# Performance work log

Measured on AMD Instinct MI355X. Metric: run time of the kernel, lower is better.

## Reference

```python
import jax, jax.numpy as jnp
import numpy as np

N_NODES = 100000


def setup_inputs() -> dict:
    key = jax.random.key(0)
    ks = jax.random.split(key, 8)
    N, E, D_IN, D_OUT = N_NODES, 1600000, 64, 64
    return {
        "emb_src": jax.random.normal(ks[0], (N, D_IN), dtype=jnp.float32),
        "emb_dst": jax.random.normal(ks[1], (N, D_IN), dtype=jnp.float32),
        "edge_weight": jax.random.uniform(ks[2], (E,), dtype=jnp.float32),
        "W": jax.random.normal(ks[3], (D_IN, D_OUT), dtype=jnp.float32) / np.sqrt(D_IN),
        "b": jnp.zeros((D_OUT,), dtype=jnp.float32),
        "src_idx": jax.random.randint(ks[4], (E,), 0, N),
        "dst_idx": jax.random.randint(ks[5], (E,), 0, N),
        "user_indices": jax.random.randint(ks[6], (N,), 0, 1000000),
        "labels": jax.random.randint(ks[7], (N,), 0, 2),
        "perm": jnp.arange(N),
    }


def reference(emb_src, emb_dst, edge_weight, W, b, src_idx, dst_idx, user_indices, labels, perm):
    # DGL update_all(u_mul_e('embedding','weight','m'), sum('m','ft')):
    # gather source embeddings, scale by edge weight, scatter-sum into dst.
    msgs = emb_src[src_idx] * edge_weight[:, None]            # [E, D]
    ft = jax.ops.segment_sum(msgs, dst_idx, num_segments=N_NODES)  # [N, D]
    # aggregate == 'SUM': self embedding + aggregated neighborhood
    h = emb_dst + ft                                          # [N, D]
    # per-row np.where(itemlist == dst_ID) matching -> permutation gather
    users = user_indices[perm]
    labs = labels[perm]
    # last layer: tanh(Linear(h)) (dropout p=0 is identity)
    item_embeddings = jnp.tanh(h @ W + b)                     # [N, D_OUT]
    return item_embeddings, users, labs
```

## Files before the change

### kernel.cpp

```cpp
#include <hip/hip_runtime.h>
#include <hip/hip_fp16.h>

#define D 64
#define NQ (D / 4)
#define NB 512
#define NPB 196
#define LOCAL_BITS 8
#define LOCAL_MASK 255
#define SCAN_W 512
#define CAP 4096
#define CAPB 3584
#define SCATTER_BLKS 256
#define FRONT_BLKS 2048

#define HACC_STRIDE 17
#define SMEM_BYTES (D * D * 4 + NPB * HACC_STRIDE * 16)

__device__ __forceinline__ float fast_tanh(float x) {
    float e = __expf(2.0f * x);
    return 1.0f - 2.0f / (e + 1.0f);
}

struct f8 { float4 a, b; };

__global__ __launch_bounds__(512) void init_cursor_kernel(int* __restrict__ cursor)
{
    int t = threadIdx.x;
    if (t < NB) cursor[t] = t * CAPB;
}

__global__ __launch_bounds__(1024) void front2_kernel(
    const int* __restrict__ src_idx,
    const int* __restrict__ dst_idx,
    const float* __restrict__ edge_weight,
    int* __restrict__ cursor,
    int2* __restrict__ payload,
    const int* __restrict__ user_indices,
    const int* __restrict__ labels,
    const int* __restrict__ perm,
    const float* __restrict__ emb_src,
    __half* __restrict__ emb_h,
    float* __restrict__ users_out,
    float* __restrict__ labs_out,
    int n_edges, int chunk, int n_nodes)
{
    const int tid = threadIdx.x;

    if (blockIdx.x < SCATTER_BLKS) {
        __shared__ int hist[NB];
        __shared__ int blockbase[NB];
        __shared__ int cur[NB];
        int lo = blockIdx.x * chunk;
        int hi = min(n_edges, lo + chunk);

        for (int i = tid; i < NB; i += 1024) { hist[i] = 0; cur[i] = 0; }
        __syncthreads();
        for (int e = lo + tid; e < hi; e += 1024)
            atomicAdd(&hist[(unsigned)dst_idx[e] / NPB], 1);
        __syncthreads();
        for (int i = tid; i < NB; i += 1024) {
            int c = hist[i];
            blockbase[i] = c ? atomicAdd(&cursor[i], c) : 0;
        }
        __syncthreads();
        for (int e = lo + tid; e < hi; e += 1024) {
            int d = dst_idx[e];
            unsigned bkt = (unsigned)d / NPB;
            int pos = blockbase[bkt] + atomicAdd(&cur[bkt], 1);
            if (pos < (int)(bkt + 1) * CAPB)
                payload[pos] = make_int2((src_idx[e] << LOCAL_BITS) | (d - (int)bkt * NPB),
                                         __float_as_int(edge_weight[e]));
        }
    } else {
        const int nblk = gridDim.x - SCATTER_BLKS;
        const int gstride = nblk * 1024;
        const int t0 = (blockIdx.x - SCATTER_BLKS) * 1024 + tid;
        for (int i = t0; i < n_nodes; i += gstride) {
            int p = perm[i];
            users_out[i] = (float)user_indices[p];
            labs_out[i]  = (float)labels[p];
        }
        const int n_cvt = n_nodes * NQ;
        for (int i = t0; i < n_cvt; i += gstride) {
            float4 v = reinterpret_cast<const float4*>(emb_src)[i];
            __half2 a, b;
            a.x = __float2half_rn(v.x); a.y = __float2half_rn(v.y);
            b.x = __float2half_rn(v.z); b.y = __float2half_rn(v.w);
            uint2 u;
            u.x = *reinterpret_cast<unsigned*>(&a);
            u.y = *reinterpret_cast<unsigned*>(&b);
            reinterpret_cast<uint2*>(emb_h)[i] = u;
        }
    }
}

template <bool USE_H, bool FIXED_BASE>
__global__ __launch_bounds__(1024, 8) void fused_gather_gemm_kernel(
    const float* __restrict__ emb_src,
    const __half* __restrict__ emb_h,
    const float* __restrict__ emb_dst,
    const float* __restrict__ Wmat,
    const float* __restrict__ bias,
    const int2* __restrict__ payload,
    const int* __restrict__ base_or_cursor,
    const int* __restrict__ counts,
    float* __restrict__ out,
    int n_nodes)
{
    __shared__ __align__(16) char smem[SMEM_BYTES];
    float*  Ws     = reinterpret_cast<float*>(smem);
    float4* Hacc   = reinterpret_cast<float4*>(smem + D * D * 4);
    int2*   sedges = reinterpret_cast<int2*>(smem + D * D * 4);
    int*    cnt    = reinterpret_cast<int*>(smem + D * D * 4 + CAP * 8);
    int*    scn    = cnt + 256;
    int*    cur    = scn + 256;

    const int tid = threadIdx.x;
    const int b   = blockIdx.x;
    int start, end;
    if constexpr (FIXED_BASE) {
        start = b * CAPB;
        end   = min(base_or_cursor[b], start + CAPB);
    } else {
        start = base_or_cursor[b];
        end   = start + counts[b];
    }

    const int g8 = tid >> 3;
    const int q8 = tid & 7;
    const float4* esrc = reinterpret_cast<const float4*>(emb_src);

    reinterpret_cast<float4*>(Ws)[tid] = reinterpret_cast<const float4*>(Wmat)[tid];

    float4 accA[2], accB[2];
    #pragma unroll
    for (int k = 0; k < 2; ++k) {
        accA[k] = make_float4(0.f, 0.f, 0.f, 0.f);
        accB[k] = make_float4(0.f, 0.f, 0.f, 0.f);
    }

    for (int cbase = start; cbase < end; cbase += CAP) {
        const int m = min(end - cbase, CAP);

        for (int i = tid; i < 256; i += 1024) { cnt[i] = 0; cur[i] = 0; }
        __syncthreads();

        int2 pe[4];
        #pragma unroll
        for (int j = 0; j < 4; ++j) {
            int i = cbase + tid + j * 1024;
            if (tid + j * 1024 < m) {
                pe[j] = payload[i];
                atomicAdd(&cnt[pe[j].x & LOCAL_MASK], 1);
            }
        }
        __syncthreads();

        if (tid < 256) scn[tid] = cnt[tid];
        __syncthreads();
        #pragma unroll
        for (int d = 1; d < 256; d <<= 1) {
            int x = 0;
            if (tid < 256 && tid >= d) x = scn[tid - d];
            __syncthreads();
            if (tid < 256) scn[tid] += x;
            __syncthreads();
        }
        if (tid < 256) scn[tid] -= cnt[tid];
        __syncthreads();

        #pragma unroll
        for (int j = 0; j < 4; ++j) {
            if (tid + j * 1024 < m) {
                int local = pe[j].x & LOCAL_MASK;
                int pos = scn[local] + atomicAdd(&cur[local], 1);
                sedges[pos] = pe[j];
            }
        }
        __syncthreads();

        #pragma unroll
        for (int k = 0; k < 2; ++k) {
            int n = g8 + 128 * k;
            if (n < NPB) {
                int mm = cnt[n];
                int bs = scn[n];
                if (mm <= 0) continue;
                int lim = mm - 1;
                float4 aA = accA[k], aB = accB[k];

                if constexpr (USE_H) {
                    int2 e0 = sedges[bs];
                    int2 e1 = sedges[bs + min(1, lim)];
                    int2 e2 = sedges[bs + min(2, lim)];
                    int2 e3 = sedges[bs + min(3, lim)];
                    uint4 u0 = *reinterpret_cast<const uint4*>(
                        emb_h + ((size_t)((unsigned)e0.x >> LOCAL_BITS) << 6) + (q8 << 3));
                    uint4 u1 = *reinterpret_cast<const uint4*>(
                        emb_h + ((size_t)((unsigned)e1.x >> LOCAL_BITS) << 6) + (q8 << 3));
                    uint4 u2 = *reinterpret_cast<const uint4*>(
                        emb_h + ((size_t)((unsigned)e2.x >> LOCAL_BITS) << 6) + (q8 << 3));
                    uint4 u3 = *reinterpret_cast<const uint4*>(
                        emb_h + ((size_t)((unsigned)e3.x >> LOCAL_BITS) << 6) + (q8 << 3));

                    for (int j = 0; j < mm; j += 4) {
                        int jn = j + 4;
                        int2 f0 = sedges[bs + min(jn,     lim)];
                        int2 f1 = sedges[bs + min(jn + 1, lim)];
                        int2 f2 = sedges[bs + min(jn + 2, lim)];
                        int2 f3 = sedges[bs + min(jn + 3, lim)];
                        uint4 w0v = *reinterpret_cast<const uint4*>(
                            emb_h + ((size_t)((unsigned)f0.x >> LOCAL_BITS) << 6) + (q8 << 3));
                        uint4 w1v = *reinterpret_cast<const uint4*>(
                            emb_h + ((size_t)((unsigned)f1.x >> LOCAL_BITS) << 6) + (q8 << 3));
                        uint4 w2v = *reinterpret_cast<const uint4*>(
                            emb_h + ((size_t)((unsigned)f2.x >> LOCAL_BITS) << 6) + (q8 << 3));
                        uint4 w3v = *reinterpret_cast<const uint4*>(
                            emb_h + ((size_t)((unsigned)f3.x >> LOCAL_BITS) << 6) + (q8 << 3));

                        float w0 = __int_as_float(e0.y);
                        float w1 = (j + 1 < mm) ? __int_as_float(e1.y) : 0.f;
                        float w2 = (j + 2 < mm) ? __int_as_float(e2.y) : 0.f;
                        float w3 = (j + 3 < mm) ? __int_as_float(e3.y) : 0.f;
                        {
                            union { uint4 u; __half2 h2[4]; } c0{u0}, c1{u1}, c2{u2}, c3{u3};
                            float2 p00 = __half22float2(c0.h2[0]), p01 = __half22float2(c0.h2[1]);
                            float2 p02 = __half22float2(c0.h2[2]), p03 = __half22float2(c0.h2[3]);
                            float2 p10 = __half22float2(c1.h2[0]), p11 = __half22float2(c1.h2[1]);
                            float2 p12 = __half22float2(c1.h2[2]), p13 = __half22float2(c1.h2[3]);
                            float2 p20 = __half22float2(c2.h2[0]), p21 = __half22float2(c2.h2[1]);
                            float2 p22 = __half22float2(c2.h2[2]), p23 = __half22float2(c2.h2[3]);
                            float2 p30 = __half22float2(c3.h2[0]), p31 = __half22float2(c3.h2[1]);
                            float2 p32 = __half22float2(c3.h2[2]), p33 = __half22float2(c3.h2[3]);
                            aA.x += p00.x * w0 + p10.x * w1 + p20.x * w2 + p30.x * w3;
                            aA.y += p00.y * w0 + p10.y * w1 + p20.y * w2 + p30.y * w3;
                            aA.z += p01.x * w0 + p11.x * w1 + p21.x * w2 + p31.x * w3;
                            aA.w += p01.y * w0 + p11.y * w1 + p21.y * w2 + p31.y * w3;
                            aB.x += p02.x * w0 + p12.x * w1 + p22.x * w2 + p32.x * w3;
                            aB.y += p02.y * w0 + p12.y * w1 + p22.y * w2 + p32.y * w3;
                            aB.z += p03.x * w0 + p13.x * w1 + p23.x * w2 + p33.x * w3;
                            aB.w += p03.y * w0 + p13.y * w1 + p23.y * w2 + p33.y * w3;
                        }
                        e0 = f0; e1 = f1; e2 = f2; e3 = f3;
                        u0 = w0v; u1 = w1v; u2 = w2v; u3 = w3v;
                    }
                } else {
                    for (int j = 0; j < mm; j += 4) {
                        int2 e0 = sedges[bs + j];
                        int2 e1 = sedges[bs + min(j + 1, lim)];
                        int2 e2 = sedges[bs + min(j + 2, lim)];
                        int2 e3 = sedges[bs + min(j + 3, lim)];
                        const float4* p0 = esrc + (size_t)((unsigned)e0.x >> LOCAL_BITS) * NQ + (q8 << 1);
                        const float4* p1 = esrc + (size_t)((unsigned)e1.x >> LOCAL_BITS) * NQ + (q8 << 1);
                        const float4* p2 = esrc + (size_t)((unsigned)e2.x >> LOCAL_BITS) * NQ + (q8 << 1);
                        const float4* p3 = esrc + (size_t)((unsigned)e3.x >> LOCAL_BITS) * NQ + (q8 << 1);
                        float4 a0 = p0[0], b0 = p0[1], a1 = p1[0], b1 = p1[1];
                        float4 a2 = p2[0], b2 = p2[1], a3 = p3[0], b3 = p3[1];
                        float w0 = __int_as_float(e0.y);
                        float w1 = (j + 1 < mm) ? __int_as_float(e1.y) : 0.f;
                        float w2 = (j + 2 < mm) ? __int_as_float(e2.y) : 0.f;
                        float w3 = (j + 3 < mm) ? __int_as_float(e3.y) : 0.f;
                        aA.x += a0.x * w0 + a1.x * w1 + a2.x * w2 + a3.x * w3;
                        aA.y += a0.y * w0 + a1.y * w1 + a2.y * w2 + a3.y * w3;
                        aA.z += a0.z * w0 + a1.z * w1 + a2.z * w2 + a3.z * w3;
                        aA.w += a0.w * w0 + a1.w * w1 + a2.w * w2 + a3.w * w3;
                        aB.x += b0.x * w0 + b1.x * w1 + b2.x * w2 + b3.x * w3;
                        aB.y += b0.y * w0 + b1.y * w1 + b2.y * w2 + b3.y * w3;
                        aB.z += b0.z * w0 + b1.z * w1 + b2.z * w2 + b3.z * w3;
                        aB.w += b0.w * w0 + b1.w * w1 + b2.w * w2 + b3.w * w3;
                    }
                }
                accA[k] = aA; accB[k] = aB;
            }
        }
        __syncthreads();
    }

    const int node0 = b * NPB;
    #pragma unroll
    for (int k = 0; k < 2; ++k) {
        int n = g8 + 128 * k;
        if (n < NPB) {
            int node = node0 + n;
            float4 d0 = make_float4(0.f, 0.f, 0.f, 0.f);
            float4 d1 = make_float4(0.f, 0.f, 0.f, 0.f);
            if (node < n_nodes) {
                const float4* ed = reinterpret_cast<const float4*>(emb_dst)
                                 + (size_t)node * NQ + (q8 << 1);
                d0 = ed[0]; d1 = ed[1];
            }
            float4 aA = accA[k], aB = accB[k];
            aA.x += d0.x; aA.y += d0.y; aA.z += d0.z; aA.w += d0.w;
            aB.x += d1.x; aB.y += d1.y; aB.z += d1.z; aB.w += d1.w;
            Hacc[n * HACC_STRIDE + (q8 << 1)]     = aA;
            Hacc[n * HACC_STRIDE + (q8 << 1) + 1] = aB;
        }
    }
    __syncthreads();

    const int g = tid >> 4;
    const int q = tid & 15;
    const float4* Ws4 = reinterpret_cast<const float4*>(Ws);
    float4 bv = reinterpret_cast<const float4*>(bias)[q];
    #pragma unroll
    for (int k = 0; k < 4; ++k) {
        int n = g + 64 * k;
        int node = node0 + n;
        if (n < NPB && node < n_nodes) {
            float4 a = make_float4(0.f, 0.f, 0.f, 0.f);
            #pragma unroll 4
            for (int kk = 0; kk < 16; ++kk) {
                float4 hv = Hacc[n * HACC_STRIDE + kk];
                float4 w0 = Ws4[(4 * kk + 0) * 16 + q];
                float4 w1 = Ws4[(4 * kk + 1) * 16 + q];
                float4 w2 = Ws4[(4 * kk + 2) * 16 + q];
                float4 w3 = Ws4[(4 * kk + 3) * 16 + q];
                a.x += hv.x * w0.x + hv.y * w1.x + hv.z * w2.x + hv.w * w3.x;
                a.y += hv.x * w0.y + hv.y * w1.y + hv.z * w2.y + hv.w * w3.y;
                a.z += hv.x * w0.z + hv.y * w1.z + hv.z * w2.z + hv.w * w3.z;
                a.w += hv.x * w0.w + hv.y * w1.w + hv.z * w2.w + hv.w * w3.w;
            }
            float4 o;
            o.x = fast_tanh(a.x + bv.x);
            o.y = fast_tanh(a.y + bv.y);
            o.z = fast_tanh(a.z + bv.z);
            o.w = fast_tanh(a.w + bv.w);
            reinterpret_cast<float4*>(out)[(size_t)node * NQ + q] = o;
        }
    }
}

__global__ __launch_bounds__(256) void meta_kernel(
    const int* __restrict__ user_indices,
    const int* __restrict__ labels,
    const int* __restrict__ perm,
    const float* __restrict__ emb_src,
    __half* __restrict__ emb_h,
    float* __restrict__ users_out,
    float* __restrict__ labs_out,
    int* __restrict__ counts,
    int n_zero,
    int n_nodes)
{
    const int stride = gridDim.x * blockDim.x;
    int t0 = blockIdx.x * blockDim.x + threadIdx.x;
    if (counts)
        for (int i = t0; i < n_zero; i += stride) counts[i] = 0;
    for (int i = t0; i < n_nodes; i += stride) {
        int p = perm[i];
        users_out[i] = (float)user_indices[p];
        labs_out[i]  = (float)labels[p];
    }
    if (emb_h) {
        const int n_cvt = n_nodes * NQ;
        for (int i = t0; i < n_cvt; i += stride) {
            float4 v = reinterpret_cast<const float4*>(emb_src)[i];
            __half2 a, b;
            a.x = __float2half_rn(v.x); a.y = __float2half_rn(v.y);
            b.x = __float2half_rn(v.z); b.y = __float2half_rn(v.w);
            uint2 u;
            u.x = *reinterpret_cast<unsigned*>(&a);
            u.y = *reinterpret_cast<unsigned*>(&b);
            reinterpret_cast<uint2*>(emb_h)[i] = u;
        }
    }
}

__global__ __launch_bounds__(1024) void hist_bucket_kernel(
    const int* __restrict__ dst_idx,
    int* __restrict__ counts,
    int n_edges, int chunk)
{
    __shared__ int hist[NB];
    for (int i = threadIdx.x; i < NB; i += 1024) hist[i] = 0;
    __syncthreads();
    int lo = blockIdx.x * chunk;
    int hi = min(n_edges, lo + chunk);
    for (int e = lo + threadIdx.x; e < hi; e += 1024)
        atomicAdd(&hist[(unsigned)dst_idx[e] / NPB], 1);
    __syncthreads();
    for (int i = threadIdx.x; i < NB; i += 1024)
        if (hist[i]) atomicAdd(&counts[i], hist[i]);
}

__global__ __launch_bounds__(SCAN_W) void scan_small_kernel(
    const int* __restrict__ counts,
    int* __restrict__ base,
    int* __restrict__ cursor,
    int nb)
{
    __shared__ int s[SCAN_W];
    int t = threadIdx.x;
    int v = (t < nb) ? counts[t] : 0;
    s[t] = v;
    __syncthreads();
    #pragma unroll
    for (int d = 1; d < SCAN_W; d <<= 1) {
        int x = (t >= d) ? s[t - d] : 0;
        __syncthreads();
        s[t] += x;
        __syncthreads();
    }
    if (t < nb) { base[t] = s[t] - v; cursor[t] = s[t] - v; }
}

__global__ __launch_bounds__(1024) void scatter_bucket_kernel(
    const int* __restrict__ src_idx,
    const int* __restrict__ dst_idx,
    const float* __restrict__ edge_weight,
    int* __restrict__ cursor,
    int2* __restrict__ payload,
    int n_edges, int chunk)
{
    __shared__ int hist[NB];
    __shared__ int blockbase[NB];
    __shared__ int cur[NB];
    const int tid = threadIdx.x;
    int lo = blockIdx.x * chunk;
    int hi = min(n_edges, lo + chunk);

    for (int i = tid; i < NB; i += 1024) { hist[i] = 0; cur[i] = 0; }
    __syncthreads();
    for (int e = lo + tid; e < hi; e += 1024)
        atomicAdd(&hist[(unsigned)dst_idx[e] / NPB], 1);
    __syncthreads();
    for (int i = tid; i < NB; i += 1024) {
        int c = hist[i];
        blockbase[i] = c ? atomicAdd(&cursor[i], c) : 0;
    }
    __syncthreads();
    for (int e = lo + tid; e < hi; e += 1024) {
        int d = dst_idx[e];
        unsigned bkt = (unsigned)d / NPB;
        int pos = blockbase[bkt] + atomicAdd(&cur[bkt], 1);
        payload[pos] = make_int2((src_idx[e] << LOCAL_BITS) | (d - (int)bkt * NPB),
                                 __float_as_int(edge_weight[e]));
    }
}

__global__ __launch_bounds__(256) void init_h_kernel(
    const float* __restrict__ emb_dst, float* __restrict__ h, int n_nodes)
{
    const int stride = gridDim.x * blockDim.x;
    const int total4 = n_nodes * NQ;
    for (int i = blockIdx.x * blockDim.x + threadIdx.x; i < total4; i += stride)
        reinterpret_cast<float4*>(h)[i] = reinterpret_cast<const float4*>(emb_dst)[i];
}

__global__ __launch_bounds__(256) void scatter_kernel(
    const float* __restrict__ emb_src,
    const float* __restrict__ edge_weight,
    const int* __restrict__ src_idx,
    const int* __restrict__ dst_idx,
    float* __restrict__ h,
    int n_edges)
{
    int t = blockIdx.x * blockDim.x + threadIdx.x;
    if (t >= n_edges * NQ) return;
    int e = t >> 4;
    int q = t & 15;
    int s = src_idx[e];
    int d = dst_idx[e];
    float w = edge_weight[e];
    float4 v = reinterpret_cast<const float4*>(emb_src)[(size_t)s * NQ + q];
    float* p = h + (size_t)d * D + q * 4;
    atomicAdd(p + 0, v.x * w);
    atomicAdd(p + 1, v.y * w);
    atomicAdd(p + 2, v.z * w);
    atomicAdd(p + 3, v.w * w);
}

__global__ __launch_bounds__(256, 4) void gemm_tanh_kernel(
    float* __restrict__ h,
    const float* __restrict__ W,
    const float* __restrict__ b,
    int n_nodes)
{
    __shared__ float Ws[D * D];
    __shared__ float Hs[64 * D];

    const int tid = threadIdx.x;

    for (int i = tid; i < D * D / 4; i += 256)
        reinterpret_cast<float4*>(Ws)[i] = reinterpret_cast<const float4*>(W)[i];

    const int tile0 = blockIdx.x * 64;

    for (int i = tid; i < 64 * NQ; i += 256) {
        int row = i >> 4;
        int kq  = i & 15;
        float4 v = make_float4(0.f, 0.f, 0.f, 0.f);
        if (tile0 + row < n_nodes)
            v = reinterpret_cast<const float4*>(h)[(size_t)(tile0 + row) * NQ + kq];
        int kqs = kq ^ ((row >> 2) & 3);
        *reinterpret_cast<float4*>(&Hs[row * D + kqs * 4]) = v;
    }
    __syncthreads();

    const int rbase = (tid >> 4) << 2;
    const int j0    = (tid & 15) << 2;

    float acc[4][4];
    #pragma unroll
    for (int r = 0; r < 4; ++r)
        #pragma unroll
        for (int j = 0; j < 4; ++j) acc[r][j] = 0.f;

    #pragma unroll 4
    for (int kq = 0; kq < 16; ++kq) {
        float4 hv[4];
        #pragma unroll
        for (int r = 0; r < 4; ++r) {
            int row = rbase + r;
            hv[r] = *reinterpret_cast<const float4*>(
                &Hs[row * D + ((kq ^ ((row >> 2) & 3)) << 2)]);
        }
        float4 wv[4];
        #pragma unroll
        for (int kk = 0; kk < 4; ++kk)
            wv[kk] = *reinterpret_cast<const float4*>(&Ws[(kq * 4 + kk) * D + j0]);
        #pragma unroll
        for (int r = 0; r < 4; ++r) {
            acc[r][0] += hv[r].x * wv[0].x + hv[r].y * wv[1].x + hv[r].z * wv[2].x + hv[r].w * wv[3].x;
            acc[r][1] += hv[r].x * wv[0].y + hv[r].y * wv[1].y + hv[r].z * wv[2].y + hv[r].w * wv[3].y;
            acc[r][2] += hv[r].x * wv[0].z + hv[r].y * wv[1].z + hv[r].z * wv[2].z + hv[r].w * wv[3].z;
            acc[r][3] += hv[r].x * wv[0].w + hv[r].y * wv[1].w + hv[r].z * wv[2].w + hv[r].w * wv[3].w;
        }
    }

    float4 bv = *reinterpret_cast<const float4*>(&b[j0]);
    #pragma unroll
    for (int r = 0; r < 4; ++r) {
        int row = tile0 + rbase + r;
        if (row < n_nodes) {
            float4 o;
            o.x = fast_tanh(acc[r][0] + bv.x);
            o.y = fast_tanh(acc[r][1] + bv.y);
            o.z = fast_tanh(acc[r][2] + bv.z);
            o.w = fast_tanh(acc[r][3] + bv.w);
            reinterpret_cast<float4*>(h)[(size_t)row * NQ + (j0 >> 2)] = o;
        }
    }
}

extern "C" void kernel_launch(void* const* d_in, const int* in_sizes, int n_in,
                              void* d_out, int out_size, void* d_ws, size_t ws_size,
                              hipStream_t stream)
{
    const float* emb_src      = (const float*)d_in[0];
    const float* emb_dst      = (const float*)d_in[1];
    const float* edge_weight  = (const float*)d_in[2];
    const float* W            = (const float*)d_in[3];
    const float* b            = (const float*)d_in[4];
    const int*   src_idx      = (const int*)d_in[5];
    const int*   dst_idx      = (const int*)d_in[6];
    const int*   user_indices = (const int*)d_in[7];
    const int*   labels       = (const int*)d_in[8];
    const int*   perm         = (const int*)d_in[9];

    const int n_nodes = in_sizes[7];
    const int n_edges = in_sizes[2];

    float* out       = (float*)d_out;
    float* h         = out;
    float* users_out = out + (size_t)n_nodes * D;
    float* labs_out  = users_out + n_nodes;

    const int nb = (n_nodes + NPB - 1) / NPB;
    const int chunk = (n_edges + SCATTER_BLKS - 1) / SCATTER_BLKS;

    size_t need_fast = (size_t)NB * 4 + 16 + (size_t)NB * CAPB * 8 + 16
                     + (size_t)n_nodes * D * 2;
    size_t need_sort = (size_t)NB * 4 * 3 + 16 + (size_t)n_edges * 8;
    size_t need_h    = need_sort + 16 + (size_t)n_nodes * D * 2;

    bool shape_ok = (nb <= NB) && (n_nodes <= (1 << (31 - LOCAL_BITS)));
    bool ok_fast  = shape_ok && (ws_size >= need_fast) &&
                    ((size_t)n_edges <= (size_t)NB * CAPB);
    bool ok_sort  = shape_ok && (ws_size >= need_sort);
    bool ok_h     = ok_sort && (ws_size >= need_h);

    if (ok_fast) {
        int*  cursor  = (int*)d_ws;
        int2* payload = (int2*)(((uintptr_t)(cursor + NB) + 15) & ~(uintptr_t)15);
        __half* emb_h = (__half*)(((uintptr_t)(payload + (size_t)NB * CAPB) + 15) & ~(uintptr_t)15);

        init_cursor_kernel<<<1, 512, 0, stream>>>(cursor);
        front2_kernel<<<FRONT_BLKS, 1024, 0, stream>>>(
            src_idx, dst_idx, edge_weight, cursor, payload,
            user_indices, labels, perm, emb_src, emb_h,
            users_out, labs_out, n_edges, chunk, n_nodes);
        fused_gather_gemm_kernel<true, true><<<nb, 1024, 0, stream>>>(
            emb_src, emb_h, emb_dst, W, b, payload, cursor, nullptr, out, n_nodes);
    } else if (ok_sort) {
        int*  counts  = (int*)d_ws;
        int*  base    = counts + NB;
        int*  cursor  = base + NB;
        int2* payload = (int2*)(((uintptr_t)(cursor + NB) + 15) & ~(uintptr_t)15);
        __half* emb_h = ok_h ? (__half*)(((uintptr_t)(payload + n_edges) + 15) & ~(uintptr_t)15)
                             : nullptr;
        const int chunk2 = (n_edges + 255) / 256;

        meta_kernel<<<1024, 256, 0, stream>>>(user_indices, labels, perm,
                                              emb_src, emb_h,
                                              users_out, labs_out, counts, NB, n_nodes);
        hist_bucket_kernel<<<256, 1024, 0, stream>>>(dst_idx, counts, n_edges, chunk2);
        scan_small_kernel<<<1, SCAN_W, 0, stream>>>(counts, base, cursor, nb);
        scatter_bucket_kernel<<<256, 1024, 0, stream>>>(
            src_idx, dst_idx, edge_weight, cursor, payload, n_edges, chunk2);
        if (ok_h)
            fused_gather_gemm_kernel<true, false><<<nb, 1024, 0, stream>>>(
                emb_src, emb_h, emb_dst, W, b, payload, base, counts, out, n_nodes);
        else
            fused_gather_gemm_kernel<false, false><<<nb, 1024, 0, stream>>>(
                emb_src, nullptr, emb_dst, W, b, payload, base, counts, out, n_nodes);
    } else {
        meta_kernel<<<512, 256, 0, stream>>>(user_indices, labels, perm,
                                             emb_src, nullptr,
                                             users_out, labs_out, nullptr, 0, n_nodes);
        init_h_kernel<<<2048, 256, 0, stream>>>(emb_dst, h, n_nodes);
        scatter_kernel<<<(n_edges * NQ + 255) / 256, 256, 0, stream>>>(
            emb_src, edge_weight, src_idx, dst_idx, h, n_edges);
        gemm_tanh_kernel<<<(n_nodes + 63) / 64, 256, 0, stream>>>(h, W, b, n_nodes);
    }
}
```

Baseline: 80.68 us.

## Interleave two nodes' gather loops and retune scatter blocks and launch bounds

The fp16 gather path now processes both of a thread-group's nodes in one merged loop, issuing eight independent row loads per iteration instead of four with software prefetch. Padding iterations are clamped to a valid source row and masked with zero weight. SCATTER_BLKS doubles and the launch-bounds occupancy hint drops from 8 to 4, which gives the compiler more registers for the wider loop. The aim is more memory-level parallelism per thread to hide gather latency, at the cost of wasted loads when the two nodes' degrees differ and possibly lower occupancy.

```diff
diff --git a/kernel.cpp b/kernel.cpp
--- a/kernel.cpp
+++ b/kernel.cpp
@@ -10,7 +10,7 @@
 #define SCAN_W 512
 #define CAP 4096
 #define CAPB 3584
-#define SCATTER_BLKS 256
+#define SCATTER_BLKS 512
 #define FRONT_BLKS 2048
 
 #define HACC_STRIDE 17
@@ -20,8 +20,6 @@
     float e = __expf(2.0f * x);
     return 1.0f - 2.0f / (e + 1.0f);
 }
-
-struct f8 { float4 a, b; };
 
 __global__ __launch_bounds__(512) void init_cursor_kernel(int* __restrict__ cursor)
 {
@@ -95,7 +93,7 @@
 }
 
 template <bool USE_H, bool FIXED_BASE>
-__global__ __launch_bounds__(1024, 8) void fused_gather_gemm_kernel(
+__global__ __launch_bounds__(1024, 4) void fused_gather_gemm_kernel(
     const float* __restrict__ emb_src,
     const __half* __restrict__ emb_h,
     const float* __restrict__ emb_dst,
@@ -128,6 +126,7 @@
 
     const int g8 = tid >> 3;
     const int q8 = tid & 7;
+    const unsigned src_max = (unsigned)(n_nodes - 1);
     const float4* esrc = reinterpret_cast<const float4*>(emb_src);
 
     reinterpret_cast<float4*>(Ws)[tid] = reinterpret_cast<const float4*>(Wmat)[tid];
@@ -179,81 +178,102 @@
         }
         __syncthreads();
 
-        #pragma unroll
-        for (int k = 0; k < 2; ++k) {
-            int n = g8 + 128 * k;
-            if (n < NPB) {
-                int mm = cnt[n];
-                int bs = scn[n];
-                if (mm <= 0) continue;
-                int lim = mm - 1;
-                float4 aA = accA[k], aB = accB[k];
-
-                if constexpr (USE_H) {
-                    int2 e0 = sedges[bs];
-                    int2 e1 = sedges[bs + min(1, lim)];
-                    int2 e2 = sedges[bs + min(2, lim)];
-                    int2 e3 = sedges[bs + min(3, lim)];
-                    uint4 u0 = *reinterpret_cast<const uint4*>(
-                        emb_h + ((size_t)((unsigned)e0.x >> LOCAL_BITS) << 6) + (q8 << 3));
-                    uint4 u1 = *reinterpret_cast<const uint4*>(
-                        emb_h + ((size_t)((unsigned)e1.x >> LOCAL_BITS) << 6) + (q8 << 3));
-                    uint4 u2 = *reinterpret_cast<const uint4*>(
-                        emb_h + ((size_t)((unsigned)e2.x >> LOCAL_BITS) << 6) + (q8 << 3));
-                    uint4 u3 = *reinterpret_cast<const uint4*>(
-                        emb_h + ((size_t)((unsigned)e3.x >> LOCAL_BITS) << 6) + (q8 << 3));
-
+        {
+            const int n0 = g8;
+            const int n1 = g8 + 128;
+            int mm0 = cnt[n0];
+            int bs0 = scn[n0];
+            int mm1 = (n1 < NPB) ? cnt[n1] : 0;
+            int bs1 = (n1 < NPB) ? scn[n1] : 0;
+            int lim0 = max(mm0 - 1, 0);
+            int lim1 = max(mm1 - 1, 0);
+            int rounds = max(mm0, mm1);
+
+            float4 aA0 = accA[0], aB0 = accB[0];
+            float4 aA1 = accA[1], aB1 = accB[1];
+
+            if constexpr (USE_H) {
+                for (int j = 0; j < rounds; j += 4) {
+                    int2 e00 = sedges[bs0 + min(j,     lim0)];
+                    int2 e01 = sedges[bs0 + min(j + 1, lim0)];
+                    int2 e02 = sedges[bs0 + min(j + 2, lim0)];
+                    int2 e03 = sedges[bs0 + min(j + 3, lim0)];
+                    int2 e10 = sedges[bs1 + min(j,     lim1)];
+                    int2 e11 = sedges[bs1 + min(j + 1, lim1)];
+                    int2 e12 = sedges[bs1 + min(j + 2, lim1)];
+                    int2 e13 = sedges[bs1 + min(j + 3, lim1)];
+                    uint4 u00 = *reinterpret_cast<const uint4*>(
+                        emb_h + ((size_t)min((unsigned)e00.x >> LOCAL_BITS, src_max) << 6) + (q8 << 3));
+                    uint4 u01 = *reinterpret_cast<const uint4*>(
+                        emb_h + ((size_t)min((unsigned)e01.x >> LOCAL_BITS, src_max) << 6) + (q8 << 3));
+                    uint4 u02 = *reinterpret_cast<const uint4*>(
+                        emb_h + ((size_t)min((unsigned)e02.x >> LOCAL_BITS, src_max) << 6) + (q8 << 3));
+                    uint4 u03 = *reinterpret_cast<const uint4*>(
+                        emb_h + ((size_t)min((unsigned)e03.x >> LOCAL_BITS, src_max) << 6) + (q8 << 3));
+                    uint4 u10 = *reinterpret_cast<const uint4*>(
+                        emb_h + ((size_t)min((unsigned)e10.x >> LOCAL_BITS, src_max) << 6) + (q8 << 3));
+                    uint4 u11 = *reinterpret_cast<const uint4*>(
+                        emb_h + ((size_t)min((unsigned)e11.x >> LOCAL_BITS, src_max) << 6) + (q8 << 3));
+                    uint4 u12 = *reinterpret_cast<const uint4*>(
+                        emb_h + ((size_t)min((unsigned)e12.x >> LOCAL_BITS, src_max) << 6) + (q8 << 3));
+                    uint4 u13 = *reinterpret_cast<const uint4*>(
+                        emb_h + ((size_t)min((unsigned)e13.x >> LOCAL_BITS, src_max) << 6) + (q8 << 3));
+
+                    float w00 = (j     < mm0) ? __int_as_float(e00.y) : 0.f;
+                    float w01 = (j + 1 < mm0) ? __int_as_float(e01.y) : 0.f;
+                    float w02 = (j + 2 < mm0) ? __int_as_float(e02.y) : 0.f;
+                    float w03 = (j + 3 < mm0) ? __int_as_float(e03.y) : 0.f;
+                    float w10 = (j     < mm1) ? __int_as_float(e10.y) : 0.f;
+                    float w11 = (j + 1 < mm1) ? __int_as_float(e11.y) : 0.f;
+                    float w12 = (j + 2 < mm1) ? __int_as_float(e12.y) : 0.f;
+                    float w13 = (j + 3 < mm1) ? __int_as_float(e13.y) : 0.f;
+
+                    union U { uint4 u; __half2 h2[4]; };
+                    U c00{u00}, c01{u01}, c02{u02}, c03{u03};
+                    U c10{u10}, c11{u11}, c12{u12}, c13{u13};
+                    #define ACC8(aA, aB, c0, c1, c2, c3, w0, w1, w2, w3)                       \
+                    {                                                                          \
+                        float2 p0a = __half22float2(c0.h2[0]), p0b = __half22float2(c0.h2[1]); \
+                        float2 p0c = __half22float2(c0.h2[2]), p0d = __half22float2(c0.h2[3]); \
+                        float2 p1a = __half22float2(c1.h2[0]), p1b = __half22float2(c1.h2[1]); \
+                        float2 p1c = __half22float2(c1.h2[2]), p1d = __half22float2(c1.h2[3]); \
+                        float2 p2a = __half22float2(c2.h2[0]), p2b = __half22float2(c2.h2[1]); \
+                        float2 p2c = __half22float2(c2.h2[2]), p2d = __half22float2(c2.h2[3]); \
+                        float2 p3a = __half22float2(c3.h2[0]), p3b = __half22float2(c3.h2[1]); \
+                        float2 p3c = __half22float2(c3.h2[2]), p3d = __half22float2(c3.h2[3]); \
+                        aA.x += p0a.x * w0 + p1a.x * w1 + p2a.x * w2 + p3a.x * w3;             \
+                        aA.y += p0a.y * w0 + p1a.y * w1 + p2a.y * w2 + p3a.y * w3;             \
+                        aA.z += p0b.x * w0 + p1b.x * w1 + p2b.x * w2 + p3b.x * w3;             \
+                        aA.w += p0b.y * w0 + p1b.y * w1 + p2b.y * w2 + p3b.y * w3;             \
+                        aB.x += p0c.x * w0 + p1c.x * w1 + p2c.x * w2 + p3c.x * w3;             \
+                        aB.y += p0c.y * w0 + p1c.y * w1 + p2c.y * w2 + p3c.y * w3;             \
+                        aB.z += p0d.x * w0 + p1d.x * w1 + p2d.x * w2 + p3d.x * w3;             \
+                        aB.w += p0d.y * w0 + p1d.y * w1 + p2d.y * w2 + p3d.y * w3;             \
+                    }
+                    ACC8(aA0, aB0, c00, c01, c02, c03, w00, w01, w02, w03)
+                    ACC8(aA1, aB1, c10, c11, c12, c13, w10, w11, w12, w13)
+                    #undef ACC8
+                }
+            } else {
+                #pragma unroll
+                for (int k = 0; k < 2; ++k) {
+                    int n = g8 + 128 * k;
+                    if (n >= NPB) continue;
+                    int mm = cnt[n];
+                    int bs = scn[n];
+                    if (mm <= 0) continue;
+                    int lim = mm - 1;
+                    float4 aA = (k == 0) ? aA0 : aA1;
+                    float4 aB = (k == 0) ? aB0 : aB1;
                     for (int j = 0; j < mm; j += 4) {
-                        int jn = j + 4;
-                        int2 f0 = sedges[bs + min(jn,     lim)];
-                        int2 f1 = sedges[bs + min(jn + 1, lim)];
-                        int2 f2 = sedges[bs + min(jn + 2, lim)];
-                        int2 f3 = sedges[bs + min(jn + 3, lim)];
-                        uint4 w0v = *reinterpret_cast<const uint4*>(
-                            emb_h + ((size_t)((unsigned)f0.x >> LOCAL_BITS) << 6) + (q8 << 3));
-                        uint4 w1v = *reinterpret_cast<const uint4*>(
-                            emb_h + ((size_t)((unsigned)f1.x >> LOCAL_BITS) << 6) + (q8 << 3));
-                        uint4 w2v = *reinterpret_cast<const uint4*>(
-                            emb_h + ((size_t)((unsigned)f2.x >> LOCAL_BITS) << 6) + (q8 << 3));
-                        uint4 w3v = *reinterpret_cast<const uint4*>(
-                            emb_h + ((size_t)((unsigned)f3.x >> LOCAL_BITS) << 6) + (q8 << 3));
-
-                        float w0 = __int_as_float(e0.y);
-                        float w1 = (j + 1 < mm) ? __int_as_float(e1.y) : 0.f;
-                        float w2 = (j + 2 < mm) ? __int_as_float(e2.y) : 0.f;
-                        float w3 = (j + 3 < mm) ? __int_as_float(e3.y) : 0.f;
-                        {
-                            union { uint4 u; __half2 h2[4]; } c0{u0}, c1{u1}, c2{u2}, c3{u3};
-                            float2 p00 = __half22float2(c0.h2[0]), p01 = __half22float2(c0.h2[1]);
-                            float2 p02 = __half22float2(c0.h2[2]), p03 = __half22float2(c0.h2[3]);
-                            float2 p10 = __half22float2(c1.h2[0]), p11 = __half22float2(c1.h2[1]);
-                            float2 p12 = __half22float2(c1.h2[2]), p13 = __half22float2(c1.h2[3]);
-                            float2 p20 = __half22float2(c2.h2[0]), p21 = __half22float2(c2.h2[1]);
-                            float2 p22 = __half22float2(c2.h2[2]), p23 = __half22float2(c2.h2[3]);
-                            float2 p30 = __half22float2(c3.h2[0]), p31 = __half22float2(c3.h2[1]);
-                            float2 p32 = __half22float2(c3.h2[2]), p33 = __half22float2(c3.h2[3]);
-                            aA.x += p00.x * w0 + p10.x * w1 + p20.x * w2 + p30.x * w3;
-                            aA.y += p00.y * w0 + p10.y * w1 + p20.y * w2 + p30.y * w3;
-                            aA.z += p01.x * w0 + p11.x * w1 + p21.x * w2 + p31.x * w3;
-                            aA.w += p01.y * w0 + p11.y * w1 + p21.y * w2 + p31.y * w3;
-                            aB.x += p02.x * w0 + p12.x * w1 + p22.x * w2 + p32.x * w3;
-                            aB.y += p02.y * w0 + p12.y * w1 + p22.y * w2 + p32.y * w3;
-                            aB.z += p03.x * w0 + p13.x * w1 + p23.x * w2 + p33.x * w3;
-                            aB.w += p03.y * w0 + p13.y * w1 + p23.y * w2 + p33.y * w3;
-                        }
-                        e0 = f0; e1 = f1; e2 = f2; e3 = f3;
-                        u0 = w0v; u1 = w1v; u2 = w2v; u3 = w3v;
-                    }
-                } else {
-                    for (int j = 0; j < mm; j += 4) {
-                        int2 e0 = sedges[bs + j];
+                        int2 e0 = sedges[bs + min(j,     lim)];
                         int2 e1 = sedges[bs + min(j + 1, lim)];
                         int2 e2 = sedges[bs + min(j + 2, lim)];
                         int2 e3 = sedges[bs + min(j + 3, lim)];
-                        const float4* p0 = esrc + (size_t)((unsigned)e0.x >> LOCAL_BITS) * NQ + (q8 << 1);
-                        const float4* p1 = esrc + (size_t)((unsigned)e1.x >> LOCAL_BITS) * NQ + (q8 << 1);
-                        const float4* p2 = esrc + (size_t)((unsigned)e2.x >> LOCAL_BITS) * NQ + (q8 << 1);
-                        const float4* p3 = esrc + (size_t)((unsigned)e3.x >> LOCAL_BITS) * NQ + (q8 << 1);
+                        const float4* p0 = esrc + (size_t)min((unsigned)e0.x >> LOCAL_BITS, src_max) * NQ + (q8 << 1);
+                        const float4* p1 = esrc + (size_t)min((unsigned)e1.x >> LOCAL_BITS, src_max) * NQ + (q8 << 1);
+                        const float4* p2 = esrc + (size_t)min((unsigned)e2.x >> LOCAL_BITS, src_max) * NQ + (q8 << 1);
+                        const float4* p3 = esrc + (size_t)min((unsigned)e3.x >> LOCAL_BITS, src_max) * NQ + (q8 << 1);
                         float4 a0 = p0[0], b0 = p0[1], a1 = p1[0], b1 = p1[1];
                         float4 a2 = p2[0], b2 = p2[1], a3 = p3[0], b3 = p3[1];
                         float w0 = __int_as_float(e0.y);
@@ -269,9 +289,11 @@
                         aB.z += b0.z * w0 + b1.z * w1 + b2.z * w2 + b3.z * w3;
                         aB.w += b0.w * w0 + b1.w * w1 + b2.w * w2 + b3.w * w3;
                     }
+                    if (k == 0) { aA0 = aA; aB0 = aB; } else { aA1 = aA; aB1 = aB; }
                 }
-                accA[k] = aA; accB[k] = aB;
             }
+            accA[0] = aA0; accB[0] = aB0;
+            accA[1] = aA1; accB[1] = aB1;
         }
         __syncthreads();
     }
```

Result: slower. 96.77 us (+19.9%).
